# Kernel optimization log

Hardware: AMD Instinct MI355X
Metric: run time of the kernel (lower is better)

Reference implementation:

```python
import jax, jax.numpy as jnp
import numpy as np

B, S, E = 4, 4096, 1024
H, D, L = 16, 64, 64   # heads, head_dim, landmarks
KS = 33                # depthwise conv kernel size (seq dim)
N_ITER = 6


def setup_inputs() -> dict:
    key = jax.random.key(0)
    ks = jax.random.split(key, 8)
    s = 0.02
    return {
        "hidden_states": jax.random.normal(ks[0], (B, S, E), dtype=jnp.float32),
        "Wq": jax.random.normal(ks[1], (E, E), dtype=jnp.float32) * s,
        "bq": jnp.zeros((E,), dtype=jnp.float32),
        "Wk": jax.random.normal(ks[2], (E, E), dtype=jnp.float32) * s,
        "bk": jnp.zeros((E,), dtype=jnp.float32),
        "Wv": jax.random.normal(ks[3], (E, E), dtype=jnp.float32) * s,
        "bv": jnp.zeros((E,), dtype=jnp.float32),
        "conv_w": jax.random.normal(ks[4], (H, 1, KS, 1), dtype=jnp.float32) * 0.1,
    }


def _iterative_pinv_original(a, n_iter=N_ITER):
    # a: [B,H,L,L]. Faithful to _pinv_original_nystrom: GLOBAL max over all batches/heads.
    eye = jnp.eye(a.shape[-1], dtype=a.dtype)
    val = a.swapaxes(-1, -2) / jnp.max(jnp.sum(a, axis=-2))
    for _ in range(n_iter):
        kv = a @ val
        val = 0.25 * val @ (13.0 * eye - kv @ (15.0 * eye - kv @ (7.0 * eye - kv)))
    return val


def reference(hidden_states, Wq, bq, Wk, bk, Wv, bv, conv_w):
    scale = D ** -0.25  # divide q and k each by head_dim**0.25

    def heads(x):  # [B,S,E] -> [B,H,S,D]
        return x.reshape(B, S, H, D).transpose(0, 2, 1, 3)

    q = heads(hidden_states @ Wq + bq) * scale
    k = heads(hidden_states @ Wk + bk) * scale
    v = heads(hidden_states @ Wv + bv)

    # landmark means over segments of length S//L
    ql = q.reshape(B, H, L, S // L, D).mean(axis=-2)  # [B,H,L,D]
    kl = k.reshape(B, H, L, S // L, D).mean(axis=-2)  # [B,H,L,D]

    kernel_1 = jax.nn.softmax(jnp.einsum('bhsd,bhld->bhsl', q, kl), axis=-1)   # [B,H,S,L]
    kernel_2 = jax.nn.softmax(jnp.einsum('bhmd,bhld->bhml', ql, kl), axis=-1)  # [B,H,L,L]
    kernel_3 = jax.nn.softmax(jnp.einsum('bhld,bhsd->bhls', ql, k), axis=-1)   # [B,H,L,S]

    pinv = _iterative_pinv_original(kernel_2)
    attention_probs = kernel_1 @ pinv            # [B,H,S,L]
    new_value = kernel_3 @ v                     # [B,H,L,D]
    ctx = attention_probs @ new_value            # [B,H,S,D]

    # depthwise conv skip on value_layer: Conv2d(H,H,(KS,1),groups=H,bias=False)
    pad = KS // 2
    conv_out = jax.lax.conv_general_dilated(
        v, conv_w, window_strides=(1, 1), padding=((pad, pad), (0, 0)),
        dimension_numbers=('NCHW', 'OIHW', 'NCHW'), feature_group_count=H)
    ctx = ctx + conv_out

    return ctx.transpose(0, 2, 1, 3).reshape(B, S, H * D)
```

## Files before the change

### kernel.cpp

```cpp
#include <hip/hip_runtime.h>
#include <stdint.h>

typedef unsigned short u16;
typedef float f32x4 __attribute__((ext_vector_type(4)));
typedef __bf16 bf16x8 __attribute__((ext_vector_type(8)));
typedef u16 u16x8 __attribute__((ext_vector_type(8)));
typedef u16 u16x4 __attribute__((ext_vector_type(4)));

#define SCALE_QK 0.35355339059327373f

#define BAR() asm volatile("s_barrier" ::: "memory")
#define WAIT_LGKM0() do { asm volatile("s_waitcnt lgkmcnt(0)" ::: "memory"); __builtin_amdgcn_sched_barrier(0); } while (0)
#define WAIT_VM(n) do { asm volatile("s_waitcnt vmcnt(" #n ")" ::: "memory"); __builtin_amdgcn_sched_barrier(0); } while (0)

__device__ __forceinline__ u16 f2bf(float f) {
  union { float f; uint32_t u; } x; x.f = f;
  uint32_t r = x.u + 0x7fffu + ((x.u >> 16) & 1u);
  return (u16)(r >> 16);
}
__device__ __forceinline__ float bf2f(u16 h) {
  union { uint32_t u; float f; } x; x.u = ((uint32_t)h) << 16;
  return x.f;
}
__device__ __forceinline__ void gload16(const void* g, void* l) {
  __builtin_amdgcn_global_load_lds((const __attribute__((address_space(1))) void*)g,
                                   (__attribute__((address_space(3))) void*)l, 16, 0, 0);
}
__device__ __forceinline__ bf16x8 ld_f32_to_bf8(const float* p) {
  f32x4 a = *(const f32x4*)p, b = *(const f32x4*)(p + 4);
  union { u16x8 u; bf16x8 h; } c;
  c.u[0] = f2bf(a[0]); c.u[1] = f2bf(a[1]); c.u[2] = f2bf(a[2]); c.u[3] = f2bf(a[3]);
  c.u[4] = f2bf(b[0]); c.u[5] = f2bf(b[1]); c.u[6] = f2bf(b[2]); c.u[7] = f2bf(b[3]);
  return c.h;
}

__global__ __launch_bounds__(256) void k_wt(const float* __restrict__ Wq, const float* __restrict__ Wk,
                                            const float* __restrict__ Wv, u16* __restrict__ Wt) {
  __shared__ float tile[64][65];
  const int bx = blockIdx.x;
  const int w = bx >> 8, tn = (bx >> 4) & 15, tk = bx & 15;
  const float* W = (w == 0) ? Wq : ((w == 1) ? Wk : Wv);
  const int t = threadIdx.x;
  const int r = t >> 2, c0 = (t & 3) * 16;
  const float* src = W + (size_t)(tk * 64 + r) * 1024 + tn * 64 + c0;
#pragma unroll
  for (int j = 0; j < 16; j += 4) {
    f32x4 x = *(const f32x4*)(src + j);
    tile[r][c0 + j + 0] = x[0]; tile[r][c0 + j + 1] = x[1];
    tile[r][c0 + j + 2] = x[2]; tile[r][c0 + j + 3] = x[3];
  }
  __syncthreads();
  u16* dst = Wt + (size_t)(w * 1024 + tn * 64 + r) * 1024 + tk * 64 + c0;
#pragma unroll
  for (int j = 0; j < 16; ++j) dst[j] = f2bf(tile[c0 + j][r]);
}

__global__ __launch_bounds__(256) void k_hb(const float* __restrict__ in, u16* __restrict__ out) {
  const size_t i = ((size_t)blockIdx.x * 256 + threadIdx.x) * 8;
  f32x4 v0 = *(const f32x4*)(in + i);
  f32x4 v1 = *(const f32x4*)(in + i + 4);
  u16x8 o;
  o[0] = f2bf(v0[0]); o[1] = f2bf(v0[1]); o[2] = f2bf(v0[2]); o[3] = f2bf(v0[3]);
  o[4] = f2bf(v1[0]); o[5] = f2bf(v1[1]); o[6] = f2bf(v1[2]); o[7] = f2bf(v1[3]);
  *(u16x8*)(out + i) = o;
}

__device__ __forceinline__ bf16x8 frg(const u16* buf, int row, int ks, int lhi) {
  const int ck = (ks << 2) + lhi;
  return *reinterpret_cast<const bf16x8*>(buf + (row << 6) + ((ck ^ (row & 7)) << 3));
}
__device__ __forceinline__ void issue(const u16* g, int rowbase, int tc, u16* ldsbase, int wid) {
  gload16(g + (((size_t)rowbase) << 10) + tc, ldsbase + ((rowbase + (wid << 3)) << 6));
}
template <int Q>
__device__ __forceinline__ void quad_mfma(const bf16x8 (&af)[2][2], const bf16x8 (&bf)[4][2],
                                          f32x4 (&acc)[8][4]) {
#pragma unroll
  for (int mm = 0; mm < 2; ++mm)
#pragma unroll
    for (int n = 0; n < 4; ++n) {
      acc[Q * 2 + mm][n] = __builtin_amdgcn_mfma_f32_16x16x32_bf16(af[mm][0], bf[n][0], acc[Q * 2 + mm][n], 0, 0, 0);
      acc[Q * 2 + mm][n] = __builtin_amdgcn_mfma_f32_16x16x32_bf16(af[mm][1], bf[n][1], acc[Q * 2 + mm][n], 0, 0, 0);
    }
}
#define LOADA(Q)                                             \
  af[0][0] = frg(ASr, rA0 + (Q)*32, 0, lhi);                 \
  af[0][1] = frg(ASr, rA0 + (Q)*32, 1, lhi);                 \
  af[1][0] = frg(ASr, rA0 + (Q)*32 + 16, 0, lhi);            \
  af[1][1] = frg(ASr, rA0 + (Q)*32 + 16, 1, lhi);

__global__ __launch_bounds__(512) void k_gemm2(const u16* __restrict__ A, const u16* __restrict__ Bt,
                                               const float* __restrict__ bq, const float* __restrict__ bk,
                                               const float* __restrict__ bv,
                                               u16* __restrict__ oq, u16* __restrict__ ok, u16* __restrict__ ov) {
  __shared__ __align__(16) u16 AS[2][256 * 64];
  __shared__ __align__(16) u16 BS[2][256 * 64];
  __shared__ __align__(16) u16 obuf[8][16][70];
  const int t = threadIdx.x, lane = t & 63, wid = t >> 6;
  const int wm = wid >> 2, wn = wid & 3;
  const int bm = blockIdx.x, bn = blockIdx.y;
  const int l15 = lane & 15, lhi = lane >> 4;

  const int rowoff = t >> 3;
  const int cswz = (t & 7) ^ (rowoff & 7);
  const u16* aG = A + (((size_t)(bm * 256 + rowoff)) << 10) + (cswz << 3);
  const u16* bG = Bt + (((size_t)(bn * 256 + rowoff)) << 10) + (cswz << 3);

  const int rA0 = wm * 128 + l15;
  const int rB0 = wn * 64 + l15;

  f32x4 acc[8][4];
#pragma unroll
  for (int m = 0; m < 8; ++m)
#pragma unroll
    for (int n = 0; n < 4; ++n) acc[m][n] = (f32x4){0.f, 0.f, 0.f, 0.f};

  issue(bG, 0, 0, BS[0], wid);
  issue(bG, 64, 0, BS[0], wid);
  issue(bG, 128, 0, BS[0], wid);
  issue(bG, 192, 0, BS[0], wid);
  issue(aG, 0, 0, AS[0], wid);
  issue(aG, 128, 0, AS[0], wid);
  issue(aG, 64, 0, AS[0], wid);
  issue(aG, 192, 0, AS[0], wid);
  WAIT_VM(2);
  BAR();

  for (int u = 0; u < 15; ++u) {
    const int pu = u & 1;
    const u16* ASr = AS[pu];
    const u16* BSr = BS[pu];
    u16* ASw = AS[pu ^ 1];
    u16* BSw = BS[pu ^ 1];
    const int tc = (u + 1) << 6;
    bf16x8 bf[4][2];
    bf16x8 af[2][2];
#pragma unroll
    for (int n = 0; n < 4; ++n) {
      bf[n][0] = frg(BSr, rB0 + n * 16, 0, lhi);
      bf[n][1] = frg(BSr, rB0 + n * 16, 1, lhi);
    }
    LOADA(0)
    issue(bG, 0, tc, BSw, wid);
    issue(bG, 64, tc, BSw, wid);
    issue(bG, 128, tc, BSw, wid);
    issue(bG, 192, tc, BSw, wid);
    BAR();
    WAIT_LGKM0();
    __builtin_amdgcn_s_setprio(1);
    quad_mfma<0>(af, bf, acc);
    __builtin_amdgcn_s_setprio(0);
    LOADA(1)
    issue(aG, 0, tc, ASw, wid);
    issue(aG, 128, tc, ASw, wid);
    BAR();
    WAIT_LGKM0();
    __builtin_amdgcn_s_setprio(1);
    quad_mfma<1>(af, bf, acc);
    __builtin_amdgcn_s_setprio(0);
    WAIT_VM(6);
    LOADA(2)
    issue(aG, 64, tc, ASw, wid);
    issue(aG, 192, tc, ASw, wid);
    BAR();
    WAIT_LGKM0();
    __builtin_amdgcn_s_setprio(1);
    quad_mfma<2>(af, bf, acc);
    __builtin_amdgcn_s_setprio(0);
    LOADA(3)
    BAR();
    WAIT_LGKM0();
    __builtin_amdgcn_s_setprio(1);
    quad_mfma<3>(af, bf, acc);
    __builtin_amdgcn_s_setprio(0);
    WAIT_VM(2);
    BAR();
  }
  {
    const u16* ASr = AS[1];
    const u16* BSr = BS[1];
    WAIT_VM(0);
    BAR();
    bf16x8 bf[4][2];
    bf16x8 af[2][2];
#pragma unroll
    for (int n = 0; n < 4; ++n) {
      bf[n][0] = frg(BSr, rB0 + n * 16, 0, lhi);
      bf[n][1] = frg(BSr, rB0 + n * 16, 1, lhi);
    }
    LOADA(0) quad_mfma<0>(af, bf, acc);
    LOADA(1) quad_mfma<1>(af, bf, acc);
    LOADA(2) quad_mfma<2>(af, bf, acc);
    LOADA(3) quad_mfma<3>(af, bf, acc);
  }

  const int which = bn >> 2;
  const float* bias = (which == 0) ? bq : ((which == 1) ? bk : bv);
  u16* op = (which == 0) ? oq : ((which == 1) ? ok : ov);
  const float scl = (which < 2) ? SCALE_QK : 1.0f;
  const int h = ((bn & 3) << 2) + wn;
  const int rowBase2 = (bm << 8) + (wm << 7);
  const int rl = lhi << 2;
  const int srow = lane >> 2, d0 = (lane & 3) * 16;
  float bb[4];
#pragma unroll
  for (int n = 0; n < 4; ++n) bb[n] = bias[((bn & 3) << 8) + (wn << 6) + n * 16 + l15];
#pragma unroll
  for (int m = 0; m < 8; ++m) {
#pragma unroll
    for (int n = 0; n < 4; ++n)
#pragma unroll
      for (int r = 0; r < 4; ++r)
        obuf[wid][rl + r][n * 16 + l15] = f2bf((acc[m][n][r] + bb[n]) * scl);
    const int gm = rowBase2 + m * 16 + srow;
    const int b_ = gm >> 12, s = gm & 4095;
    u16* dst = op + (((size_t)b_ * 16 + h) * 4096 + s) * 64 + d0;
    *(u16x8*)dst = *(const u16x8*)&obuf[wid][srow][d0];
    *(u16x8*)(dst + 8) = *(const u16x8*)&obuf[wid][srow][d0 + 8];
  }
}

__global__ __launch_bounds__(64) void k_lm(const u16* __restrict__ q, const u16* __restrict__ k,
                                           float* __restrict__ ql, float* __restrict__ kl,
                                           u16* __restrict__ klb) {
  const int bid = blockIdx.x;
  const int d = threadIdx.x;
  const u16* qp = q + (size_t)bid * 4096 + d;
  const u16* kp = k + (size_t)bid * 4096 + d;
  float sq = 0.f, sk = 0.f;
#pragma unroll 4
  for (int m = 0; m < 64; ++m) { sq += bf2f(qp[m * 64]); sk += bf2f(kp[m * 64]); }
  const float qm = sq * 0.015625f, km = sk * 0.015625f;
  ql[(size_t)bid * 64 + d] = qm;
  kl[(size_t)bid * 64 + d] = km;
  klb[(size_t)bid * 64 + d] = f2bf(km);
}

__global__ __launch_bounds__(256) void k_k2(const float* __restrict__ ql, const float* __restrict__ kl,
                                            float* __restrict__ k2t, float* __restrict__ colmax) {
  __shared__ __align__(16) float qlT[64 * 68];
  __shared__ __align__(16) float klT[64 * 68];
  __shared__ __align__(16) float sc[64 * 68];
  const int bh = blockIdx.x, t = threadIdx.x;
  {
    const int r = t >> 2, c0 = (t & 3) * 16;
    const float* qp = ql + (size_t)bh * 4096 + r * 64 + c0;
    const float* kp = kl + (size_t)bh * 4096 + r * 64 + c0;
#pragma unroll
    for (int j = 0; j < 16; ++j) { qlT[(c0 + j) * 68 + r] = qp[j]; klT[(c0 + j) * 68 + r] = kp[j]; }
  }
  __syncthreads();
  {
    const int mg = (t >> 4) * 4, lg = (t & 15) * 4;
    float acc[4][4];
#pragma unroll
    for (int i = 0; i < 4; ++i)
#pragma unroll
      for (int j = 0; j < 4; ++j) acc[i][j] = 0.f;
    for (int d0 = 0; d0 < 64; ++d0) {
      f32x4 x = *(const f32x4*)&qlT[d0 * 68 + mg];
      f32x4 y = *(const f32x4*)&klT[d0 * 68 + lg];
#pragma unroll
      for (int i = 0; i < 4; ++i)
#pragma unroll
        for (int j = 0; j < 4; ++j) acc[i][j] += x[i] * y[j];
    }
#pragma unroll
    for (int i = 0; i < 4; ++i)
#pragma unroll
      for (int j = 0; j < 4; ++j) sc[(mg + i) * 68 + lg + j] = acc[i][j];
  }
  __syncthreads();
  if (t < 64) {
    float mx = -1e30f;
    for (int l = 0; l < 64; ++l) mx = fmaxf(mx, sc[t * 68 + l]);
    float sum = 0.f;
    for (int l = 0; l < 64; ++l) { float e = __expf(sc[t * 68 + l] - mx); sc[t * 68 + l] = e; sum += e; }
    const float inv = 1.0f / sum;
    for (int l = 0; l < 64; ++l) sc[t * 68 + l] *= inv;
  }
  __syncthreads();
  {
    const int r = t >> 2, c0 = (t & 3) * 16;
    float* ot = k2t + (size_t)bh * 4096 + r * 64 + c0;
#pragma unroll
    for (int j = 0; j < 16; ++j) ot[j] = sc[(c0 + j) * 68 + r];
  }
  if (t < 64) {
    float s = 0.f;
    for (int m = 0; m < 64; ++m) s += sc[m * 68 + t];
    for (int off = 32; off; off >>= 1) s = fmaxf(s, __shfl_down(s, off, 64));
    if (t == 0) colmax[bh] = s;
  }
}

__global__ __launch_bounds__(64) void k_max(const float* __restrict__ colmax, float* __restrict__ gmax) {
  const int t = threadIdx.x;
  float v = colmax[t];
  for (int off = 32; off; off >>= 1) v = fmaxf(v, __shfl_down(v, off, 64));
  if (t == 0) *gmax = v;
}

__global__ __launch_bounds__(512) void k_pinv(const float* __restrict__ k2t, const float* __restrict__ gmaxp,
                                              float* __restrict__ pinv) {
  __shared__ float valN[4096];
  __shared__ float kvT[4096];
  __shared__ float t1N[4096];
  __shared__ float t2N[4096];
  const int bh = blockIdx.x, t = threadIdx.x;
  const float* aT = k2t + (size_t)bh * 4096;
  const float ginv = 1.0f / gmaxp[0];
  const int rt = t >> 3, ct0 = (t & 7) * 8;
  {
    const float* p = aT + rt * 64 + ct0;
#pragma unroll
    for (int j = 0; j < 8; ++j) valN[rt * 64 + ct0 + j] = p[j] * ginv;
  }
  __syncthreads();
  const int rg = (t >> 4) * 2, cg = (t & 15) * 4;
  float acc[2][4];
  for (int it = 0; it < 6; ++it) {
#pragma unroll
    for (int i = 0; i < 2; ++i)
#pragma unroll
      for (int j = 0; j < 4; ++j) acc[i][j] = 0.f;
    for (int k = 0; k < 64; ++k) {
      const float x0 = aT[k * 64 + rg], x1 = aT[k * 64 + rg + 1];
      f32x4 y = *(const f32x4*)&valN[k * 64 + cg];
#pragma unroll
      for (int j = 0; j < 4; ++j) { acc[0][j] += x0 * y[j]; acc[1][j] += x1 * y[j]; }
    }
#pragma unroll
    for (int i = 0; i < 2; ++i)
#pragma unroll
      for (int j = 0; j < 4; ++j) kvT[(cg + j) * 64 + rg + i] = acc[i][j];
    __syncthreads();
#pragma unroll
    for (int j = 0; j < 8; ++j) {
      const int c = ct0 + j;
      t1N[rt * 64 + c] = ((rt == c) ? 7.0f : 0.0f) - kvT[c * 64 + rt];
    }
    __syncthreads();
#pragma unroll
    for (int i = 0; i < 2; ++i)
#pragma unroll
      for (int j = 0; j < 4; ++j) acc[i][j] = 0.f;
    for (int k = 0; k < 64; ++k) {
      const float x0 = kvT[k * 64 + rg], x1 = kvT[k * 64 + rg + 1];
      f32x4 y = *(const f32x4*)&t1N[k * 64 + cg];
#pragma unroll
      for (int j = 0; j < 4; ++j) { acc[0][j] += x0 * y[j]; acc[1][j] += x1 * y[j]; }
    }
#pragma unroll
    for (int i = 0; i < 2; ++i)
#pragma unroll
      for (int j = 0; j < 4; ++j) {
        const int r_ = rg + i, c_ = cg + j;
        t2N[r_ * 64 + c_] = ((r_ == c_) ? 15.0f : 0.0f) - acc[i][j];
      }
    __syncthreads();
#pragma unroll
    for (int i = 0; i < 2; ++i)
#pragma unroll
      for (int j = 0; j < 4; ++j) acc[i][j] = 0.f;
    for (int k = 0; k < 64; ++k) {
      const float x0 = kvT[k * 64 + rg], x1 = kvT[k * 64 + rg + 1];
      f32x4 y = *(const f32x4*)&t2N[k * 64 + cg];
#pragma unroll
      for (int j = 0; j < 4; ++j) { acc[0][j] += x0 * y[j]; acc[1][j] += x1 * y[j]; }
    }
#pragma unroll
    for (int i = 0; i < 2; ++i)
#pragma unroll
      for (int j = 0; j < 4; ++j) {
        const int r_ = rg + i, c_ = cg + j;
        t1N[r_ * 64 + c_] = ((r_ == c_) ? 13.0f : 0.0f) - acc[i][j];
      }
    __syncthreads();
#pragma unroll
    for (int j = 0; j < 8; ++j) t2N[(ct0 + j) * 64 + rt] = valN[rt * 64 + ct0 + j];
    __syncthreads();
#pragma unroll
    for (int i = 0; i < 2; ++i)
#pragma unroll
      for (int j = 0; j < 4; ++j) acc[i][j] = 0.f;
    for (int k = 0; k < 64; ++k) {
      const float x0 = t2N[k * 64 + rg], x1 = t2N[k * 64 + rg + 1];
      f32x4 y = *(const f32x4*)&t1N[k * 64 + cg];
#pragma unroll
      for (int j = 0; j < 4; ++j) { acc[0][j] += x0 * y[j]; acc[1][j] += x1 * y[j]; }
    }
#pragma unroll
    for (int i = 0; i < 2; ++i)
#pragma unroll
      for (int j = 0; j < 4; ++j) valN[(rg + i) * 64 + cg + j] = 0.25f * acc[i][j];
    __syncthreads();
  }
  {
    float* o = pinv + (size_t)bh * 4096 + rt * 64 + ct0;
#pragma unroll
    for (int j = 0; j < 8; ++j) o[j] = valN[rt * 64 + ct0 + j];
  }
}

__global__ __launch_bounds__(256) void k_s3nv(const float* __restrict__ ql, const u16* __restrict__ kb,
                                              const u16* __restrict__ vb,
                                              float* __restrict__ nvp, float* __restrict__ zp) {
  __shared__ __align__(16) u16 VT[64][72];
  __shared__ __align__(16) u16 e_lds[4][16][72];
  const int bh = blockIdx.x, scn = blockIdx.y;
  const int t = threadIdx.x, lane = t & 63, w = t >> 6;
  const int l15 = lane & 15, kg = (lane >> 4) << 3, rl = (lane >> 4) << 2;
  const float* aRow = ql + (size_t)bh * 4096 + (w * 16 + l15) * 64 + kg;
  bf16x8 aql[2];
  aql[0] = ld_f32_to_bf8(aRow);
  aql[1] = ld_f32_to_bf8(aRow + 32);
  f32x4 accv[4];
#pragma unroll
  for (int n = 0; n < 4; ++n) accv[n] = (f32x4){0.f, 0.f, 0.f, 0.f};
  float zacc[4] = {0.f, 0.f, 0.f, 0.f};

  for (int sub = 0; sub < 16; ++sub) {
    const int s0 = scn * 1024 + sub * 64;
    __syncthreads();
    {
      const u16* vp = vb + ((size_t)bh * 4096 + s0 + lane) * 64 + w * 16;
      u16x8 h0 = *(const u16x8*)vp, h1 = *(const u16x8*)(vp + 8);
#pragma unroll
      for (int j = 0; j < 8; ++j) { VT[w * 16 + j][lane] = h0[j]; VT[w * 16 + 8 + j][lane] = h1[j]; }
    }
    __syncthreads();
    const u16* bRow = kb + ((size_t)bh * 4096 + s0 + l15) * 64 + kg;
    f32x4 e[4];
#pragma unroll
    for (int n = 0; n < 4; ++n) e[n] = (f32x4){0.f, 0.f, 0.f, 0.f};
#pragma unroll
    for (int ks = 0; ks < 2; ++ks)
#pragma unroll
      for (int n = 0; n < 4; ++n) {
        bf16x8 bk = *reinterpret_cast<const bf16x8*>(bRow + n * 1024 + ks * 32);
        e[n] = __builtin_amdgcn_mfma_f32_16x16x32_bf16(aql[ks], bk, e[n], 0, 0, 0);
      }
#pragma unroll
    for (int n = 0; n < 4; ++n)
#pragma unroll
      for (int r = 0; r < 4; ++r) {
        const float v = __expf(e[n][r]);
        zacc[r] += v;
        e_lds[w][rl + r][n * 16 + l15] = f2bf(v);
      }
    WAIT_LGKM0();
#pragma unroll
    for (int ks = 0; ks < 2; ++ks) {
      bf16x8 af = *reinterpret_cast<const bf16x8*>(&e_lds[w][l15][kg + ks * 32]);
#pragma unroll
      for (int n = 0; n < 4; ++n) {
        bf16x8 bf_ = *reinterpret_cast<const bf16x8*>(&VT[n * 16 + l15][kg + ks * 32]);
        accv[n] = __builtin_amdgcn_mfma_f32_16x16x32_bf16(af, bf_, accv[n], 0, 0, 0);
      }
    }
  }
#pragma unroll
  for (int r = 0; r < 4; ++r)
#pragma unroll
    for (int n = 0; n < 4; ++n)
      nvp[(((size_t)scn * 64 + bh) * 64 + w * 16 + rl + r) * 64 + n * 16 + l15] = accv[n][r];
#pragma unroll
  for (int r = 0; r < 4; ++r) {
    float s = zacc[r];
    s += __shfl_xor(s, 1, 64); s += __shfl_xor(s, 2, 64);
    s += __shfl_xor(s, 4, 64); s += __shfl_xor(s, 8, 64);
    if (l15 == 0) zp[((size_t)scn * 64 + bh) * 64 + w * 16 + rl + r] = s;
  }
}

__global__ __launch_bounds__(256) void k_pnv(const float* __restrict__ pinv, const float* __restrict__ nvp,
                                             const float* __restrict__ zp, u16* __restrict__ Mtb) {
  __shared__ __align__(16) float XT[64 * 68];
  __shared__ __align__(16) float Y[64 * 68];
  const int bh = blockIdx.x, t = threadIdx.x;
  {
    const int r = t >> 2, c0 = (t & 3) * 16;
    const float* pp = pinv + (size_t)bh * 4096 + r * 64 + c0;
#pragma unroll
    for (int j = 0; j < 16; ++j) XT[(c0 + j) * 68 + r] = pp[j];
    float zs = 0.f;
#pragma unroll
    for (int p = 0; p < 4; ++p) zs += zp[((size_t)p * 64 + bh) * 64 + r];
    const float iz = 1.0f / zs;
#pragma unroll
    for (int j = 0; j < 16; ++j) {
      float s = 0.f;
#pragma unroll
      for (int p = 0; p < 4; ++p) s += nvp[(((size_t)p * 64 + bh) * 64 + r) * 64 + c0 + j];
      Y[r * 68 + c0 + j] = s * iz;
    }
  }
  __syncthreads();
  const int rg = (t >> 4) * 4, cg = (t & 15) * 4;
  float acc[4][4];
#pragma unroll
  for (int i = 0; i < 4; ++i)
#pragma unroll
    for (int j = 0; j < 4; ++j) acc[i][j] = 0.f;
  for (int k = 0; k < 64; ++k) {
    f32x4 x = *(const f32x4*)&XT[k * 68 + rg];
    f32x4 y = *(const f32x4*)&Y[k * 68 + cg];
#pragma unroll
    for (int i = 0; i < 4; ++i)
#pragma unroll
      for (int j = 0; j < 4; ++j) acc[i][j] += x[i] * y[j];
  }
#pragma unroll
  for (int j = 0; j < 4; ++j) {
    u16x4 o = {f2bf(acc[0][j]), f2bf(acc[1][j]), f2bf(acc[2][j]), f2bf(acc[3][j])};
    *(u16x4*)&Mtb[(size_t)bh * 4096 + (cg + j) * 64 + rg] = o;
  }
}

__global__ __launch_bounds__(256) void k_out(const u16* __restrict__ qb, const u16* __restrict__ vb,
                                             const u16* __restrict__ klb, const u16* __restrict__ Mtb,
                                             const float* __restrict__ cw, float* __restrict__ out) {
  __shared__ __align__(16) u16 P_lds[4][16][72];
  __shared__ __align__(16) u16 vtile_t[64][100];
  __shared__ float wsh[33];
  const int bid = blockIdx.x;
  const int bh = bid >> 6, st = bid & 63;
  const int b = bh >> 4, h = bh & 15;
  const int t = threadIdx.x, lane = t & 63, w = t >> 6;
  const int sbase = st * 64;
  const int l15 = lane & 15, kg = (lane >> 4) << 3, rl = (lane >> 4) << 2;

  if (t < 33) wsh[t] = cw[h * 33 + t];
  for (int idx = t; idx < 96 * 8; idx += 256) {
    const int row = idx >> 3, c8 = idx & 7;
    const int sg = sbase + row - 16;
    u16x8 val = {0, 0, 0, 0, 0, 0, 0, 0};
    if (sg >= 0 && sg < 4096) val = *(const u16x8*)(vb + ((size_t)bh * 4096 + sg) * 64 + c8 * 8);
#pragma unroll
    for (int j = 0; j < 8; ++j) vtile_t[c8 * 8 + j][row] = val[j];
  }

  f32x4 c1[4];
#pragma unroll
  for (int n = 0; n < 4; ++n) c1[n] = (f32x4){0.f, 0.f, 0.f, 0.f};
  {
    const u16* aRow = qb + ((size_t)bh * 4096 + sbase + w * 16 + l15) * 64 + kg;
    const u16* kRow = klb + (size_t)bh * 4096 + l15 * 64 + kg;
#pragma unroll
    for (int ks = 0; ks < 2; ++ks) {
      bf16x8 af = *reinterpret_cast<const bf16x8*>(aRow + ks * 32);
#pragma unroll
      for (int n = 0; n < 4; ++n) {
        bf16x8 bf_ = *reinterpret_cast<const bf16x8*>(kRow + n * 1024 + ks * 32);
        c1[n] = __builtin_amdgcn_mfma_f32_16x16x32_bf16(af, bf_, c1[n], 0, 0, 0);
      }
    }
  }
  float invZ[4];
  {
    float z[4] = {0.f, 0.f, 0.f, 0.f};
#pragma unroll
    for (int n = 0; n < 4; ++n)
#pragma unroll
      for (int r = 0; r < 4; ++r) { float v = __expf(c1[n][r]); c1[n][r] = v; z[r] += v; }
#pragma unroll
    for (int r = 0; r < 4; ++r) {
      float s = z[r];
      s += __shfl_xor(s, 1, 64); s += __shfl_xor(s, 2, 64);
      s += __shfl_xor(s, 4, 64); s += __shfl_xor(s, 8, 64);
      invZ[r] = 1.0f / s;
    }
#pragma unroll
    for (int n = 0; n < 4; ++n)
#pragma unroll
      for (int r = 0; r < 4; ++r)
        P_lds[w][rl + r][n * 16 + l15] = f2bf(c1[n][r]);
  }
  __syncthreads();
  f32x4 c2[4];
#pragma unroll
  for (int n = 0; n < 4; ++n) c2[n] = (f32x4){0.f, 0.f, 0.f, 0.f};
  {
    const u16* mRow = Mtb + (size_t)bh * 4096 + l15 * 64 + kg;
#pragma unroll
    for (int ks = 0; ks < 2; ++ks) {
      bf16x8 af = *reinterpret_cast<const bf16x8*>(&P_lds[w][l15][kg + ks * 32]);
#pragma unroll
      for (int n = 0; n < 4; ++n) {
        bf16x8 bf_ = *reinterpret_cast<const bf16x8*>(mRow + n * 1024 + ks * 32);
        c2[n] = __builtin_amdgcn_mfma_f32_16x16x32_bf16(af, bf_, c2[n], 0, 0, 0);
      }
    }
  }
  const int base = w * 16 + rl;
#pragma unroll
  for (int n = 0; n < 4; ++n) {
    const int d = n * 16 + l15;
    float vcol[36];
#pragma unroll
    for (int k8 = 0; k8 < 9; ++k8) {
      u16x4 vq = *(const u16x4*)&vtile_t[d][base + k8 * 4];
      vcol[k8 * 4 + 0] = bf2f(vq[0]); vcol[k8 * 4 + 1] = bf2f(vq[1]);
      vcol[k8 * 4 + 2] = bf2f(vq[2]); vcol[k8 * 4 + 3] = bf2f(vq[3]);
    }
    float cv[4] = {0.f, 0.f, 0.f, 0.f};
#pragma unroll
    for (int jt = 0; jt < 33; ++jt) {
      const float ww = wsh[jt];
#pragma unroll
      for (int r = 0; r < 4; ++r) cv[r] += ww * vcol[r + jt];
    }
#pragma unroll
    for (int r = 0; r < 4; ++r) {
      const int sgl = sbase + base + r;
      out[((size_t)b * 4096 + sgl) * 1024 + h * 64 + d] = c2[n][r] * invZ[r] + cv[r];
    }
  }
}

extern "C" void kernel_launch(void* const* d_in, const int* in_sizes, int n_in,
                              void* d_out, int out_size, void* d_ws, size_t ws_size,
                              hipStream_t stream) {
  const float* hidden = (const float*)d_in[0];
  const float* Wq = (const float*)d_in[1];
  const float* bq = (const float*)d_in[2];
  const float* Wk = (const float*)d_in[3];
  const float* bk = (const float*)d_in[4];
  const float* Wv = (const float*)d_in[5];
  const float* bv = (const float*)d_in[6];
  const float* cw = (const float*)d_in[7];
  float* out = (float*)d_out;

  char* ws = (char*)d_ws;
  u16* qb = (u16*)(ws);
  u16* kb = (u16*)(ws + 33554432ull);
  u16* vb = (u16*)(ws + 67108864ull);
  float* ql = (float*)(ws + 100663296ull);
  float* kl = (float*)(ws + 101711872ull);
  float* k2t = (float*)(ws + 102760448ull);
  float* pinvb = (float*)(ws + 103809024ull);
  float* nvp = (float*)(ws + 104857600ull);
  float* zp = (float*)(ws + 109051904ull);
  u16* Mtb = (u16*)(ws + 109117440ull);
  u16* klb = (u16*)(ws + 109641728ull);
  float* stats = (float*)(ws + 110690304ull);
  u16* wt = (u16*)(ws + 110694400ull);
  u16* hb = (u16*)(ws + 116985856ull);

  k_wt<<<768, 256, 0, stream>>>(Wq, Wk, Wv, wt);
  k_hb<<<8192, 256, 0, stream>>>(hidden, hb);
  k_gemm2<<<dim3(64, 12), 512, 0, stream>>>(hb, wt, bq, bk, bv, qb, kb, vb);
  k_lm<<<4096, 64, 0, stream>>>(qb, kb, ql, kl, klb);
  k_k2<<<64, 256, 0, stream>>>(ql, kl, k2t, stats);
  k_max<<<1, 64, 0, stream>>>(stats, stats + 64);
  k_pinv<<<64, 512, 0, stream>>>(k2t, stats + 64, pinvb);
  k_s3nv<<<dim3(64, 4), 256, 0, stream>>>(ql, kb, vb, nvp, zp);
  k_pnv<<<64, 256, 0, stream>>>(pinvb, nvp, zp, Mtb);
  k_out<<<4096, 256, 0, stream>>>(qb, vb, klb, Mtb, cw, out);
  (void)in_sizes; (void)n_in; (void)out_size; (void)ws_size;
}
```

Baseline: 318.9 us.

## Fuse landmark means into QKV GEMM epilogue and restructure main loop schedule

Landmark means for q and k are now computed from the fp32 accumulators in the QKV GEMM epilogue using cross-lane shuffles, which removes the separate k_lm kernel and its re-read of q/k. The bf16 copy of kl is now written inside k_k2. The GEMM main loop is also rescheduled: it double-buffers the A fragments, drops most intra-iteration barriers and lgkm waits, and waits for all global loads at the end of each iteration. The means now come from unrounded fp32 values, which changes numerics slightly. The fuller vmcnt(0) wait could expose load latency.

New measurement: 307.2 us. 1.04x faster.

```diff
diff --git a/kernel.cpp b/kernel.cpp
--- a/kernel.cpp
+++ b/kernel.cpp
@@ -83,16 +83,17 @@
       acc[Q * 2 + mm][n] = __builtin_amdgcn_mfma_f32_16x16x32_bf16(af[mm][1], bf[n][1], acc[Q * 2 + mm][n], 0, 0, 0);
     }
 }
-#define LOADA(Q)                                             \
-  af[0][0] = frg(ASr, rA0 + (Q)*32, 0, lhi);                 \
-  af[0][1] = frg(ASr, rA0 + (Q)*32, 1, lhi);                 \
-  af[1][0] = frg(ASr, rA0 + (Q)*32 + 16, 0, lhi);            \
-  af[1][1] = frg(ASr, rA0 + (Q)*32 + 16, 1, lhi);
+#define LOADA_TO(dst, Q)                                     \
+  dst[0][0] = frg(ASr, rA0 + (Q)*32, 0, lhi);                \
+  dst[0][1] = frg(ASr, rA0 + (Q)*32, 1, lhi);                \
+  dst[1][0] = frg(ASr, rA0 + (Q)*32 + 16, 0, lhi);           \
+  dst[1][1] = frg(ASr, rA0 + (Q)*32 + 16, 1, lhi);
 
 __global__ __launch_bounds__(512) void k_gemm2(const u16* __restrict__ A, const u16* __restrict__ Bt,
                                                const float* __restrict__ bq, const float* __restrict__ bk,
                                                const float* __restrict__ bv,
-                                               u16* __restrict__ oq, u16* __restrict__ ok, u16* __restrict__ ov) {
+                                               u16* __restrict__ oq, u16* __restrict__ ok, u16* __restrict__ ov,
+                                               float* __restrict__ ql, float* __restrict__ kl) {
   __shared__ __align__(16) u16 AS[2][256 * 64];
   __shared__ __align__(16) u16 BS[2][256 * 64];
   __shared__ __align__(16) u16 obuf[8][16][70];
@@ -123,7 +124,7 @@
   issue(aG, 128, 0, AS[0], wid);
   issue(aG, 64, 0, AS[0], wid);
   issue(aG, 192, 0, AS[0], wid);
-  WAIT_VM(2);
+  WAIT_VM(0);
   BAR();
 
   for (int u = 0; u < 15; ++u) {
@@ -133,65 +134,58 @@
     u16* ASw = AS[pu ^ 1];
     u16* BSw = BS[pu ^ 1];
     const int tc = (u + 1) << 6;
-    bf16x8 bf[4][2];
-    bf16x8 af[2][2];
+    bf16x8 bfr[4][2];
+    bf16x8 afA[2][2], afB[2][2];
 #pragma unroll
     for (int n = 0; n < 4; ++n) {
-      bf[n][0] = frg(BSr, rB0 + n * 16, 0, lhi);
-      bf[n][1] = frg(BSr, rB0 + n * 16, 1, lhi);
-    }
-    LOADA(0)
+      bfr[n][0] = frg(BSr, rB0 + n * 16, 0, lhi);
+      bfr[n][1] = frg(BSr, rB0 + n * 16, 1, lhi);
+    }
+    LOADA_TO(afA, 0)
+    LOADA_TO(afB, 1)
     issue(bG, 0, tc, BSw, wid);
     issue(bG, 64, tc, BSw, wid);
     issue(bG, 128, tc, BSw, wid);
     issue(bG, 192, tc, BSw, wid);
-    BAR();
-    WAIT_LGKM0();
-    __builtin_amdgcn_s_setprio(1);
-    quad_mfma<0>(af, bf, acc);
-    __builtin_amdgcn_s_setprio(0);
-    LOADA(1)
     issue(aG, 0, tc, ASw, wid);
     issue(aG, 128, tc, ASw, wid);
-    BAR();
-    WAIT_LGKM0();
     __builtin_amdgcn_s_setprio(1);
-    quad_mfma<1>(af, bf, acc);
+    quad_mfma<0>(afA, bfr, acc);
     __builtin_amdgcn_s_setprio(0);
-    WAIT_VM(6);
-    LOADA(2)
+    LOADA_TO(afA, 2)
     issue(aG, 64, tc, ASw, wid);
     issue(aG, 192, tc, ASw, wid);
-    BAR();
-    WAIT_LGKM0();
     __builtin_amdgcn_s_setprio(1);
-    quad_mfma<2>(af, bf, acc);
+    quad_mfma<1>(afB, bfr, acc);
     __builtin_amdgcn_s_setprio(0);
-    LOADA(3)
-    BAR();
-    WAIT_LGKM0();
+    LOADA_TO(afB, 3)
     __builtin_amdgcn_s_setprio(1);
-    quad_mfma<3>(af, bf, acc);
+    quad_mfma<2>(afA, bfr, acc);
     __builtin_amdgcn_s_setprio(0);
-    WAIT_VM(2);
+    __builtin_amdgcn_s_setprio(1);
+    quad_mfma<3>(afB, bfr, acc);
+    __builtin_amdgcn_s_setprio(0);
+    WAIT_VM(0);
     BAR();
   }
   {
     const u16* ASr = AS[1];
     const u16* BSr = BS[1];
-    WAIT_VM(0);
-    BAR();
-    bf16x8 bf[4][2];
-    bf16x8 af[2][2];
+    bf16x8 bfr[4][2];
+    bf16x8 afA[2][2], afB[2][2];
 #pragma unroll
     for (int n = 0; n < 4; ++n) {
-      bf[n][0] = frg(BSr, rB0 + n * 16, 0, lhi);
-      bf[n][1] = frg(BSr, rB0 + n * 16, 1, lhi);
-    }
-    LOADA(0) quad_mfma<0>(af, bf, acc);
-    LOADA(1) quad_mfma<1>(af, bf, acc);
-    LOADA(2) quad_mfma<2>(af, bf, acc);
-    LOADA(3) quad_mfma<3>(af, bf, acc);
+      bfr[n][0] = frg(BSr, rB0 + n * 16, 0, lhi);
+      bfr[n][1] = frg(BSr, rB0 + n * 16, 1, lhi);
+    }
+    LOADA_TO(afA, 0)
+    LOADA_TO(afB, 1)
+    quad_mfma<0>(afA, bfr, acc);
+    LOADA_TO(afA, 2)
+    quad_mfma<1>(afB, bfr, acc);
+    LOADA_TO(afB, 3)
+    quad_mfma<2>(afA, bfr, acc);
+    quad_mfma<3>(afB, bfr, acc);
   }
 
   const int which = bn >> 2;
@@ -218,26 +212,32 @@
     *(u16x8*)dst = *(const u16x8*)&obuf[wid][srow][d0];
     *(u16x8*)(dst + 8) = *(const u16x8*)&obuf[wid][srow][d0 + 8];
   }
-}
-
-__global__ __launch_bounds__(64) void k_lm(const u16* __restrict__ q, const u16* __restrict__ k,
-                                           float* __restrict__ ql, float* __restrict__ kl,
-                                           u16* __restrict__ klb) {
-  const int bid = blockIdx.x;
-  const int d = threadIdx.x;
-  const u16* qp = q + (size_t)bid * 4096 + d;
-  const u16* kp = k + (size_t)bid * 4096 + d;
-  float sq = 0.f, sk = 0.f;
-#pragma unroll 4
-  for (int m = 0; m < 64; ++m) { sq += bf2f(qp[m * 64]); sk += bf2f(kp[m * 64]); }
-  const float qm = sq * 0.015625f, km = sk * 0.015625f;
-  ql[(size_t)bid * 64 + d] = qm;
-  kl[(size_t)bid * 64 + d] = km;
-  klb[(size_t)bid * 64 + d] = f2bf(km);
+  if (which < 2) {
+    float* lmp = (which == 0) ? ql : kl;
+    const int bh = ((bm >> 4) << 4) + h;
+#pragma unroll
+    for (int sg = 0; sg < 2; ++sg) {
+#pragma unroll
+      for (int n = 0; n < 4; ++n) {
+        float s = 0.f;
+#pragma unroll
+        for (int mi = 0; mi < 4; ++mi)
+#pragma unroll
+          for (int r = 0; r < 4; ++r) s += (acc[sg * 4 + mi][n][r] + bb[n]) * scl;
+        s += __shfl_xor(s, 16, 64);
+        s += __shfl_xor(s, 32, 64);
+        if (lhi == 0) {
+          const int lseg = ((bm & 15) << 2) + (wm << 1) + sg;
+          lmp[(size_t)bh * 4096 + lseg * 64 + n * 16 + l15] = s * 0.015625f;
+        }
+      }
+    }
+  }
 }
 
 __global__ __launch_bounds__(256) void k_k2(const float* __restrict__ ql, const float* __restrict__ kl,
-                                            float* __restrict__ k2t, float* __restrict__ colmax) {
+                                            float* __restrict__ k2t, float* __restrict__ colmax,
+                                            u16* __restrict__ klb) {
   __shared__ __align__(16) float qlT[64 * 68];
   __shared__ __align__(16) float klT[64 * 68];
   __shared__ __align__(16) float sc[64 * 68];
@@ -246,8 +246,14 @@
     const int r = t >> 2, c0 = (t & 3) * 16;
     const float* qp = ql + (size_t)bh * 4096 + r * 64 + c0;
     const float* kp = kl + (size_t)bh * 4096 + r * 64 + c0;
-#pragma unroll
-    for (int j = 0; j < 16; ++j) { qlT[(c0 + j) * 68 + r] = qp[j]; klT[(c0 + j) * 68 + r] = kp[j]; }
+    u16* kb_ = klb + (size_t)bh * 4096 + r * 64 + c0;
+#pragma unroll
+    for (int j = 0; j < 16; ++j) {
+      qlT[(c0 + j) * 68 + r] = qp[j];
+      const float kv = kp[j];
+      klT[(c0 + j) * 68 + r] = kv;
+      kb_[j] = f2bf(kv);
+    }
   }
   __syncthreads();
   {
@@ -650,9 +656,8 @@
 
   k_wt<<<768, 256, 0, stream>>>(Wq, Wk, Wv, wt);
   k_hb<<<8192, 256, 0, stream>>>(hidden, hb);
-  k_gemm2<<<dim3(64, 12), 512, 0, stream>>>(hb, wt, bq, bk, bv, qb, kb, vb);
-  k_lm<<<4096, 64, 0, stream>>>(qb, kb, ql, kl, klb);
-  k_k2<<<64, 256, 0, stream>>>(ql, kl, k2t, stats);
+  k_gemm2<<<dim3(64, 12), 512, 0, stream>>>(hb, wt, bq, bk, bv, qb, kb, vb, ql, kl);
+  k_k2<<<64, 256, 0, stream>>>(ql, kl, k2t, stats, klb);
   k_max<<<1, 64, 0, stream>>>(stats, stats + 64);
   k_pinv<<<64, 512, 0, stream>>>(k2t, stats + 64, pinvb);
   k_s3nv<<<dim3(64, 4), 256, 0, stream>>>(ql, kb, vb, nvp, zp);
```
